# Performance work log

Measured on AMD Instinct MI355X. Metric: run time of the kernel, lower is better.

## Reference

```python
import jax, jax.numpy as jnp
import numpy as np

N_NODES = 100000
N_EDGES = 1600000
D_FEAT = 64
H1 = 16
H2 = 1


def setup_inputs() -> dict:
    key = jax.random.key(0)
    ks = jax.random.split(key, 8)
    x = jax.random.normal(ks[0], (N_NODES, D_FEAT), dtype=jnp.float32)
    edge_index = jax.random.randint(ks[1], (2, N_EDGES), 0, N_NODES, dtype=jnp.int64)
    s1 = 1.0 / np.sqrt(D_FEAT)
    s2 = 1.0 / np.sqrt(H1)
    Wl1 = jax.random.uniform(ks[2], (H1, D_FEAT), jnp.float32, -s1, s1)
    Wr1 = jax.random.uniform(ks[3], (H1, D_FEAT), jnp.float32, -s1, s1)
    b1 = jax.random.uniform(ks[4], (H1,), jnp.float32, -s1, s1)
    Wl2 = jax.random.uniform(ks[5], (H2, H1), jnp.float32, -s2, s2)
    Wr2 = jax.random.uniform(ks[6], (H2, H1), jnp.float32, -s2, s2)
    b2 = jax.random.uniform(ks[7], (H2,), jnp.float32, -s2, s2)
    return {"x": x, "edge_index": edge_index, "Wl1": Wl1, "Wr1": Wr1, "b1": b1,
            "Wl2": Wl2, "Wr2": Wr2, "b2": b2}


def _sage_conv(h, src, dst, Wl, Wr, b, n_nodes):
    # mean aggregation of source-node features onto destination nodes
    msg_sum = jax.ops.segment_sum(h[src], dst, num_segments=n_nodes)  # [N, d]
    cnt = jax.ops.segment_sum(jnp.ones((src.shape[0],), h.dtype), dst,
                              num_segments=n_nodes)  # [N]
    mean = msg_sum / jnp.maximum(cnt, 1.0)[:, None]
    # out = lin_l(mean_neighbors) + lin_r(self) + bias
    return mean @ Wl.T + h @ Wr.T + b


def reference(x, edge_index, Wl1, Wr1, b1, Wl2, Wr2, b2):
    src, dst = edge_index[0], edge_index[1]
    n = x.shape[0]
    h = jax.nn.relu(_sage_conv(x, src, dst, Wl1, Wr1, b1, n))
    # F.dropout(training=False) is identity at inference
    out = _sage_conv(h, src, dst, Wl2, Wr2, b2, n)
    return out
```

## Files before the change

### kernel.cpp

```cpp
#include <hip/hip_runtime.h>
#include <hip/hip_fp16.h>

#define H1F 16
#define BSH 8
#define BNODES 256
#define MAXBUCK 512
#define CAPSH 13
#define CAPB (1 << CAPSH)
#define SSH 10
#define TILE 4096
#define MAXPT 16

__global__ __launch_bounds__(512) void part_kernel(
    const int* __restrict__ ei,
    int* __restrict__ cur8,
    unsigned int* __restrict__ edge2,
    int E) {
    __shared__ int lhist[MAXBUCK];
    __shared__ int lbase[MAXBUCK];
    __shared__ int gbase[MAXBUCK];
    __shared__ int wsum[8];
    __shared__ unsigned int stage[TILE];
    __shared__ unsigned short sbuck[TILE];

    int t = threadIdx.x;
    int shard = blockIdx.x & 7;
    lhist[t] = 0;
    __syncthreads();

    int e0 = blockIdx.x * TILE;
    int eb = e0 + t * 8;

    int ss[8], dd[8];
    if (eb + 8 <= E) {
        int4 s0 = *(const int4*)(ei + eb);
        int4 s1 = *(const int4*)(ei + eb + 4);
        int4 d0 = *(const int4*)(ei + E + eb);
        int4 d1 = *(const int4*)(ei + E + eb + 4);
        ss[0]=s0.x; ss[1]=s0.y; ss[2]=s0.z; ss[3]=s0.w;
        ss[4]=s1.x; ss[5]=s1.y; ss[6]=s1.z; ss[7]=s1.w;
        dd[0]=d0.x; dd[1]=d0.y; dd[2]=d0.z; dd[3]=d0.w;
        dd[4]=d1.x; dd[5]=d1.y; dd[6]=d1.z; dd[7]=d1.w;
    } else {
#pragma unroll
        for (int k = 0; k < 8; ++k) {
            int e = eb + k;
            ss[k] = (e < E) ? ei[e] : -1;
            dd[k] = (e < E) ? ei[E + e] : 0;
        }
    }

    unsigned int pk[8];
    int rk[8], bk[8];
#pragma unroll
    for (int k = 0; k < 8; ++k) {
        if (ss[k] >= 0) {
            int b = dd[k] >> BSH;
            bk[k] = b;
            pk[k] = ((unsigned int)ss[k] << BSH) |
                    (unsigned int)(dd[k] & (BNODES - 1));
            rk[k] = atomicAdd(&lhist[b], 1);
        } else {
            bk[k] = -1;
        }
    }
    __syncthreads();

    int cnt = E - e0; if (cnt > TILE) cnt = TILE;

    int v = lhist[t];
    if (v > 0)
        gbase[t] = (t << CAPSH) + (shard << SSH) +
                   atomicAdd(&cur8[shard * MAXBUCK + t], v);
    int lane = t & 63, wid = t >> 6;
    int s = v;
#pragma unroll
    for (int d = 1; d < 64; d <<= 1) {
        int u = __shfl_up(s, d);
        if (lane >= d) s += u;
    }
    if (lane == 63) wsum[wid] = s;
    __syncthreads();
    int wofs = 0;
    for (int w = 0; w < wid; ++w) wofs += wsum[w];
    lbase[t] = wofs + s - v;
    __syncthreads();

#pragma unroll
    for (int k = 0; k < 8; ++k) {
        if (bk[k] >= 0) {
            int p = lbase[bk[k]] + rk[k];
            stage[p] = pk[k];
            sbuck[p] = (unsigned short)bk[k];
        }
    }
    __syncthreads();

    for (int i = t; i < cnt; i += 512) {
        int b = sbuck[i];
        int idx = gbase[b] + (i - lbase[b]);
        if (idx < (b << CAPSH) + ((shard + 1) << SSH)) edge2[idx] = stage[i];
    }
}

union SharedU {
    struct {
        int h[BNODES];
        int wsum[4];
    } s;
    struct {
        float4 wl4[16][17];
        float4 wr4[16][17];
    } q;
};

__global__ __launch_bounds__(512) void sortproj_kernel(
    const unsigned int* __restrict__ edge2,
    const int* __restrict__ cur8,
    int* __restrict__ csr,
    int* __restrict__ offp,
    int* __restrict__ degv,
    const float* __restrict__ x,
    const float* __restrict__ Wl1,
    const float* __restrict__ Wr1,
    const float* __restrict__ b1,
    __half* __restrict__ xl,
    float* __restrict__ xr,
    int N, int nSort) {
    __shared__ SharedU sh;
    int t = threadIdx.x;

    if ((int)blockIdx.x < nSort) {
        int b = blockIdx.x;
        int n0 = b << BSH;
        int e0 = b << CAPSH;

        if (t < BNODES) sh.s.h[t] = 0;
        __syncthreads();

        unsigned int rw[MAXPT];
#pragma unroll
        for (int s = 0; s < 8; ++s) {
            int cs = cur8[s * MAXBUCK + b];
            if (cs > (1 << SSH)) cs = (1 << SSH);
            int base = e0 + (s << SSH);
#pragma unroll
            for (int k = 0; k < 2; ++k) {
                int idx = (k << 9) + t;
                rw[s * 2 + k] = (idx < cs) ? edge2[base + idx] : 0xFFFFFFFFu;
            }
        }

#pragma unroll
        for (int k = 0; k < MAXPT; ++k)
            if (rw[k] != 0xFFFFFFFFu) atomicAdd(&sh.s.h[rw[k] & (BNODES - 1)], 1);
        __syncthreads();

        int lane = t & 63, wid = t >> 6;
        int v = 0, s = 0;
        if (t < BNODES) {
            v = sh.s.h[t];
            s = v;
#pragma unroll
            for (int d = 1; d < 64; d <<= 1) {
                int u = __shfl_up(s, d);
                if (lane >= d) s += u;
            }
            if (lane == 63) sh.s.wsum[wid] = s;
        }
        __syncthreads();
        if (t < BNODES) {
            int wofs = 0;
            for (int w = 0; w < wid; ++w) wofs += sh.s.wsum[w];
            int excl = wofs + s - v;
            int gn = n0 + t;
            if (gn < N) {
                degv[gn] = v;
                offp[gn] = e0 + excl;
            }
            sh.s.h[t] = excl;
        }
        __syncthreads();

#pragma unroll
        for (int k = 0; k < MAXPT; ++k) {
            if (rw[k] != 0xFFFFFFFFu) {
                int d = (int)(rw[k] & (BNODES - 1));
                int pos = atomicAdd(&sh.s.h[d], 1);
                csr[e0 + pos] = (int)(rw[k] >> BSH);
            }
        }
    } else {
        if (t < 256) {
            ((float4*)&sh.q.wl4[t >> 4][t & 15])[0] = ((const float4*)Wl1)[t];
        } else {
            int u = t - 256;
            ((float4*)&sh.q.wr4[u >> 4][u & 15])[0] = ((const float4*)Wr1)[u];
        }
        __syncthreads();

        int f = t & 15;
        int nl = t >> 4;
        float bf = b1[f];
        int blk = blockIdx.x - nSort;
        const float4* x4 = (const float4*)x;

#pragma unroll
        for (int rep = 0; rep < 4; ++rep) {
            int gn = blk * 128 + rep * 32 + nl;
            if (gn < N) {
                float al = 0.0f, ar = 0.0f;
#pragma unroll
                for (int k4 = 0; k4 < 16; ++k4) {
                    float4 xv = x4[(size_t)gn * 16 + k4];
                    float4 a = sh.q.wl4[f][k4];
                    float4 b = sh.q.wr4[f][k4];
                    al += xv.x * a.x + xv.y * a.y + xv.z * a.z + xv.w * a.w;
                    ar += xv.x * b.x + xv.y * b.y + xv.z * b.z + xv.w * b.w;
                }
                xl[(size_t)gn * H1F + f] = __float2half(al);
                xr[(size_t)gn * H1F + f] = ar + bf;
            }
        }
    }
}

__global__ void gather1_kernel(const int* __restrict__ csr,
                               const int* __restrict__ offp,
                               const int* __restrict__ degv,
                               const __half2* __restrict__ xl2,
                               const float2* __restrict__ xr2,
                               const float* __restrict__ Wl2,
                               const float* __restrict__ Wr2,
                               const float* __restrict__ b2,
                               float* __restrict__ hl2,
                               float* __restrict__ outp,
                               int N, int nbuck) {
    int g = blockIdx.x;
    int xcd = g & 7, r = g >> 3;
    int bi = r >> 3, k = r & 7;
    int b = bi * 8 + xcd;
    if (b >= nbuck) return;
    int node = (b << BSH) + (k << 5) + (threadIdx.x >> 3);
    int l = threadIdx.x & 7;
    if (node >= N) return;

    int d = degv[node];
    const int* row = csr + offp[node];

    float sx = 0.0f, sy = 0.0f;
    int j = 0;
    for (; j + 4 <= d; j += 4) {
        int s0 = row[j], s1 = row[j + 1], s2 = row[j + 2], s3 = row[j + 3];
        float2 v0 = __half22float2(xl2[(size_t)s0 * 8 + l]);
        float2 v1 = __half22float2(xl2[(size_t)s1 * 8 + l]);
        float2 v2 = __half22float2(xl2[(size_t)s2 * 8 + l]);
        float2 v3 = __half22float2(xl2[(size_t)s3 * 8 + l]);
        sx += v0.x + v1.x + v2.x + v3.x;
        sy += v0.y + v1.y + v2.y + v3.y;
    }
    for (; j < d; ++j) {
        float2 v = __half22float2(xl2[(size_t)row[j] * 8 + l]);
        sx += v.x; sy += v.y;
    }

    float inv = 1.0f / fmaxf((float)d, 1.0f);
    float2 xrv = xr2[(size_t)node * 8 + l];
    float h0 = fmaxf(sx * inv + xrv.x, 0.0f);
    float h1 = fmaxf(sy * inv + xrv.y, 0.0f);
    float2 wlv = ((const float2*)Wl2)[l];
    float2 wrv = ((const float2*)Wr2)[l];
    float pl = h0 * wlv.x + h1 * wlv.y;
    float pr = h0 * wrv.x + h1 * wrv.y;
#pragma unroll
    for (int off = 4; off; off >>= 1) {
        pl += __shfl_xor(pl, off);
        pr += __shfl_xor(pr, off);
    }
    if (l == 0) {
        hl2[node] = pl;
        outp[node] = pr + b2[0];
    }
}

__global__ void gather2_kernel(const int* __restrict__ csr,
                               const int* __restrict__ offp,
                               const int* __restrict__ degv,
                               const float* __restrict__ hl2,
                               const float* __restrict__ outp,
                               float* __restrict__ out,
                               int N, int nbuck) {
    int g = blockIdx.x;
    int xcd = g & 7, r = g >> 3;
    int bi = r >> 2, k = r & 3;
    int b = bi * 8 + xcd;
    if (b >= nbuck) return;
    int node = (b << BSH) + (k << 6) + (threadIdx.x >> 2);
    int l = threadIdx.x & 3;
    if (node >= N) return;

    int d = degv[node];
    const int* row = csr + offp[node];

    float s = 0.0f;
    for (int j = l; j < d; j += 4) s += hl2[row[j]];
    s += __shfl_xor(s, 1);
    s += __shfl_xor(s, 2);
    if (l == 0) out[node] = s / fmaxf((float)d, 1.0f) + outp[node];
}

extern "C" void kernel_launch(void* const* d_in, const int* in_sizes, int n_in,
                              void* d_out, int out_size, void* d_ws, size_t ws_size,
                              hipStream_t stream) {
    const float* x   = (const float*)d_in[0];
    const int*   ei  = (const int*)d_in[1];
    const float* Wl1 = (const float*)d_in[2];
    const float* Wr1 = (const float*)d_in[3];
    const float* b1  = (const float*)d_in[4];
    const float* Wl2 = (const float*)d_in[5];
    const float* Wr2 = (const float*)d_in[6];
    const float* b2  = (const float*)d_in[7];
    float* out = (float*)d_out;

    int N = in_sizes[0] / 64;
    int E = in_sizes[1] / 2;
    int nbuck = (N + BNODES - 1) >> BSH;

    size_t win = (size_t)nbuck << CAPSH;
    int* cur8 = (int*)d_ws;
    unsigned int* edge2 = (unsigned int*)(cur8 + 8 * MAXBUCK);
    int*   csr  = (int*)(edge2 + win);
    int*   offp = csr + win;
    int*   degv = offp + N;
    __half* xl  = (__half*)(degv + N);
    float* xr   = (float*)(xl + (size_t)16 * N);
    float* hl2  = xr + (size_t)16 * N;
    float* outp = hl2 + N;

    int nPart = (E + TILE - 1) / TILE;
    int nProj = (N + 127) / 128;

    (void)hipMemsetAsync(cur8, 0, 8 * MAXBUCK * sizeof(int), stream);

    part_kernel<<<nPart, 512, 0, stream>>>(ei, cur8, edge2, E);

    sortproj_kernel<<<nbuck + nProj, 512, 0, stream>>>(
        edge2, cur8, csr, offp, degv,
        x, Wl1, Wr1, b1, xl, xr, N, nbuck);

    int grid1 = 8 * ((nbuck + 7) / 8) * 8;
    gather1_kernel<<<grid1, 256, 0, stream>>>(
        csr, offp, degv, (const __half2*)xl, (const float2*)xr,
        Wl2, Wr2, b2, hl2, outp, N, nbuck);

    int grid2 = 8 * ((nbuck + 7) / 8) * 4;
    gather2_kernel<<<grid2, 256, 0, stream>>>(
        csr, offp, degv, hl2, outp, out, N, nbuck);
}
```

Baseline: 70.95 us.

## Co-schedule projection with partition and simplify gather block mapping

The dense layer-1 projection moves out of the sort kernel and into the partition kernel, so partition and projection blocks share one launch and the sort kernel runs only bucket sorting. The gather kernels drop the XCD-aware bucket swizzle, use plain linear node indexing and grow from 256 to 512 threads per block. All kernels now take a single Params struct. The shared-memory union now includes the partition staging buffers, which raises LDS use for the projection blocks, and losing the XCD locality mapping may change L2 behaviour.

```diff
diff --git a/kernel.cpp b/kernel.cpp
--- a/kernel.cpp
+++ b/kernel.cpp
@@ -6,37 +6,58 @@
 #define BNODES 256
 #define MAXBUCK 512
 #define CAPSH 13
-#define CAPB (1 << CAPSH)
 #define SSH 10
 #define TILE 4096
 #define MAXPT 16
 
-__global__ __launch_bounds__(512) void part_kernel(
-    const int* __restrict__ ei,
-    int* __restrict__ cur8,
-    unsigned int* __restrict__ edge2,
-    int E) {
-    __shared__ int lhist[MAXBUCK];
-    __shared__ int lbase[MAXBUCK];
-    __shared__ int gbase[MAXBUCK];
-    __shared__ int wsum[8];
-    __shared__ unsigned int stage[TILE];
-    __shared__ unsigned short sbuck[TILE];
-
-    int t = threadIdx.x;
-    int shard = blockIdx.x & 7;
-    lhist[t] = 0;
-    __syncthreads();
-
-    int e0 = blockIdx.x * TILE;
+struct Params {
+    const float* x;
+    const float* Wl1; const float* Wr1; const float* b1;
+    const float* Wl2; const float* Wr2; const float* b2;
+    const int* ei;
+    int* cur8;
+    unsigned int* edge2;
+    int* csr; int* offp; int* degv;
+    __half* xl; float* xr; float* hl2; float* outp;
+    float* out;
+    int N, E, nPart, nProj, nbuck;
+};
+
+union SharedU {
+    struct {
+        int lhist[MAXBUCK];
+        int lbase[MAXBUCK];
+        int gbase[MAXBUCK];
+        int wsum[8];
+        unsigned int stage[TILE];
+        unsigned short sbuck[TILE];
+    } p;
+    struct {
+        float4 wl4[16][17];
+        float4 wr4[16][17];
+    } q;
+    struct {
+        int h[BNODES];
+        int wsum[4];
+    } s;
+};
+
+__device__ __forceinline__ void do_part(const Params& P, int vb, SharedU& sh) {
+    int t = threadIdx.x;
+    int shard = vb & 7;
+    sh.p.lhist[t] = 0;
+    __syncthreads();
+
+    int E = P.E;
+    int e0 = vb * TILE;
     int eb = e0 + t * 8;
 
     int ss[8], dd[8];
     if (eb + 8 <= E) {
-        int4 s0 = *(const int4*)(ei + eb);
-        int4 s1 = *(const int4*)(ei + eb + 4);
-        int4 d0 = *(const int4*)(ei + E + eb);
-        int4 d1 = *(const int4*)(ei + E + eb + 4);
+        int4 s0 = *(const int4*)(P.ei + eb);
+        int4 s1 = *(const int4*)(P.ei + eb + 4);
+        int4 d0 = *(const int4*)(P.ei + E + eb);
+        int4 d1 = *(const int4*)(P.ei + E + eb + 4);
         ss[0]=s0.x; ss[1]=s0.y; ss[2]=s0.z; ss[3]=s0.w;
         ss[4]=s1.x; ss[5]=s1.y; ss[6]=s1.z; ss[7]=s1.w;
         dd[0]=d0.x; dd[1]=d0.y; dd[2]=d0.z; dd[3]=d0.w;
@@ -45,8 +66,8 @@
 #pragma unroll
         for (int k = 0; k < 8; ++k) {
             int e = eb + k;
-            ss[k] = (e < E) ? ei[e] : -1;
-            dd[k] = (e < E) ? ei[E + e] : 0;
+            ss[k] = (e < E) ? P.ei[e] : -1;
+            dd[k] = (e < E) ? P.ei[E + e] : 0;
         }
     }
 
@@ -59,7 +80,7 @@
             bk[k] = b;
             pk[k] = ((unsigned int)ss[k] << BSH) |
                     (unsigned int)(dd[k] & (BNODES - 1));
-            rk[k] = atomicAdd(&lhist[b], 1);
+            rk[k] = atomicAdd(&sh.p.lhist[b], 1);
         } else {
             bk[k] = -1;
         }
@@ -68,10 +89,10 @@
 
     int cnt = E - e0; if (cnt > TILE) cnt = TILE;
 
-    int v = lhist[t];
+    int v = sh.p.lhist[t];
     if (v > 0)
-        gbase[t] = (t << CAPSH) + (shard << SSH) +
-                   atomicAdd(&cur8[shard * MAXBUCK + t], v);
+        sh.p.gbase[t] = (t << CAPSH) + (shard << SSH) +
+                        atomicAdd(&P.cur8[shard * MAXBUCK + t], v);
     int lane = t & 63, wid = t >> 6;
     int s = v;
 #pragma unroll
@@ -79,174 +100,138 @@
         int u = __shfl_up(s, d);
         if (lane >= d) s += u;
     }
-    if (lane == 63) wsum[wid] = s;
+    if (lane == 63) sh.p.wsum[wid] = s;
     __syncthreads();
     int wofs = 0;
-    for (int w = 0; w < wid; ++w) wofs += wsum[w];
-    lbase[t] = wofs + s - v;
+    for (int w = 0; w < wid; ++w) wofs += sh.p.wsum[w];
+    sh.p.lbase[t] = wofs + s - v;
     __syncthreads();
 
 #pragma unroll
     for (int k = 0; k < 8; ++k) {
         if (bk[k] >= 0) {
-            int p = lbase[bk[k]] + rk[k];
-            stage[p] = pk[k];
-            sbuck[p] = (unsigned short)bk[k];
+            int p = sh.p.lbase[bk[k]] + rk[k];
+            sh.p.stage[p] = pk[k];
+            sh.p.sbuck[p] = (unsigned short)bk[k];
         }
     }
     __syncthreads();
 
     for (int i = t; i < cnt; i += 512) {
-        int b = sbuck[i];
-        int idx = gbase[b] + (i - lbase[b]);
-        if (idx < (b << CAPSH) + ((shard + 1) << SSH)) edge2[idx] = stage[i];
-    }
-}
-
-union SharedU {
-    struct {
-        int h[BNODES];
-        int wsum[4];
-    } s;
-    struct {
-        float4 wl4[16][17];
-        float4 wr4[16][17];
-    } q;
-};
-
-__global__ __launch_bounds__(512) void sortproj_kernel(
-    const unsigned int* __restrict__ edge2,
-    const int* __restrict__ cur8,
-    int* __restrict__ csr,
-    int* __restrict__ offp,
-    int* __restrict__ degv,
-    const float* __restrict__ x,
-    const float* __restrict__ Wl1,
-    const float* __restrict__ Wr1,
-    const float* __restrict__ b1,
-    __half* __restrict__ xl,
-    float* __restrict__ xr,
-    int N, int nSort) {
-    __shared__ SharedU sh;
-    int t = threadIdx.x;
-
-    if ((int)blockIdx.x < nSort) {
-        int b = blockIdx.x;
-        int n0 = b << BSH;
-        int e0 = b << CAPSH;
-
-        if (t < BNODES) sh.s.h[t] = 0;
-        __syncthreads();
-
-        unsigned int rw[MAXPT];
-#pragma unroll
-        for (int s = 0; s < 8; ++s) {
-            int cs = cur8[s * MAXBUCK + b];
-            if (cs > (1 << SSH)) cs = (1 << SSH);
-            int base = e0 + (s << SSH);
-#pragma unroll
-            for (int k = 0; k < 2; ++k) {
-                int idx = (k << 9) + t;
-                rw[s * 2 + k] = (idx < cs) ? edge2[base + idx] : 0xFFFFFFFFu;
+        int b = sh.p.sbuck[i];
+        int idx = sh.p.gbase[b] + (i - sh.p.lbase[b]);
+        int shardEnd = (b << CAPSH) + ((shard + 1) << SSH);
+        if (idx < shardEnd) P.edge2[idx] = sh.p.stage[i];
+    }
+}
+
+__device__ __forceinline__ void do_proj(const Params& P, int pvb, SharedU& sh) {
+    int t = threadIdx.x;
+    if (t < 256) {
+        sh.q.wl4[t >> 4][t & 15] = ((const float4*)P.Wl1)[t];
+    } else {
+        int u = t - 256;
+        sh.q.wr4[u >> 4][u & 15] = ((const float4*)P.Wr1)[u];
+    }
+    __syncthreads();
+
+    int f = t & 15;
+    int nl = t >> 4;
+    float bf = P.b1[f];
+    const float4* x4 = (const float4*)P.x;
+
+#pragma unroll
+    for (int rep = 0; rep < 4; ++rep) {
+        int gn = pvb * 128 + rep * 32 + nl;
+        if (gn < P.N) {
+            float al = 0.0f, ar = 0.0f;
+#pragma unroll
+            for (int k4 = 0; k4 < 16; ++k4) {
+                float4 xv = x4[(size_t)gn * 16 + k4];
+                float4 a = sh.q.wl4[f][k4];
+                float4 b = sh.q.wr4[f][k4];
+                al += xv.x * a.x + xv.y * a.y + xv.z * a.z + xv.w * a.w;
+                ar += xv.x * b.x + xv.y * b.y + xv.z * b.z + xv.w * b.w;
             }
-        }
-
-#pragma unroll
-        for (int k = 0; k < MAXPT; ++k)
-            if (rw[k] != 0xFFFFFFFFu) atomicAdd(&sh.s.h[rw[k] & (BNODES - 1)], 1);
-        __syncthreads();
-
-        int lane = t & 63, wid = t >> 6;
-        int v = 0, s = 0;
-        if (t < BNODES) {
-            v = sh.s.h[t];
-            s = v;
-#pragma unroll
-            for (int d = 1; d < 64; d <<= 1) {
-                int u = __shfl_up(s, d);
-                if (lane >= d) s += u;
-            }
-            if (lane == 63) sh.s.wsum[wid] = s;
-        }
-        __syncthreads();
-        if (t < BNODES) {
-            int wofs = 0;
-            for (int w = 0; w < wid; ++w) wofs += sh.s.wsum[w];
-            int excl = wofs + s - v;
-            int gn = n0 + t;
-            if (gn < N) {
-                degv[gn] = v;
-                offp[gn] = e0 + excl;
-            }
-            sh.s.h[t] = excl;
-        }
-        __syncthreads();
-
-#pragma unroll
-        for (int k = 0; k < MAXPT; ++k) {
-            if (rw[k] != 0xFFFFFFFFu) {
-                int d = (int)(rw[k] & (BNODES - 1));
-                int pos = atomicAdd(&sh.s.h[d], 1);
-                csr[e0 + pos] = (int)(rw[k] >> BSH);
-            }
-        }
-    } else {
-        if (t < 256) {
-            ((float4*)&sh.q.wl4[t >> 4][t & 15])[0] = ((const float4*)Wl1)[t];
-        } else {
-            int u = t - 256;
-            ((float4*)&sh.q.wr4[u >> 4][u & 15])[0] = ((const float4*)Wr1)[u];
-        }
-        __syncthreads();
-
-        int f = t & 15;
-        int nl = t >> 4;
-        float bf = b1[f];
-        int blk = blockIdx.x - nSort;
-        const float4* x4 = (const float4*)x;
-
-#pragma unroll
-        for (int rep = 0; rep < 4; ++rep) {
-            int gn = blk * 128 + rep * 32 + nl;
-            if (gn < N) {
-                float al = 0.0f, ar = 0.0f;
-#pragma unroll
-                for (int k4 = 0; k4 < 16; ++k4) {
-                    float4 xv = x4[(size_t)gn * 16 + k4];
-                    float4 a = sh.q.wl4[f][k4];
-                    float4 b = sh.q.wr4[f][k4];
-                    al += xv.x * a.x + xv.y * a.y + xv.z * a.z + xv.w * a.w;
-                    ar += xv.x * b.x + xv.y * b.y + xv.z * b.z + xv.w * b.w;
-                }
-                xl[(size_t)gn * H1F + f] = __float2half(al);
-                xr[(size_t)gn * H1F + f] = ar + bf;
-            }
-        }
-    }
-}
-
-__global__ void gather1_kernel(const int* __restrict__ csr,
-                               const int* __restrict__ offp,
-                               const int* __restrict__ degv,
-                               const __half2* __restrict__ xl2,
-                               const float2* __restrict__ xr2,
-                               const float* __restrict__ Wl2,
-                               const float* __restrict__ Wr2,
-                               const float* __restrict__ b2,
-                               float* __restrict__ hl2,
-                               float* __restrict__ outp,
-                               int N, int nbuck) {
-    int g = blockIdx.x;
-    int xcd = g & 7, r = g >> 3;
-    int bi = r >> 3, k = r & 7;
-    int b = bi * 8 + xcd;
-    if (b >= nbuck) return;
-    int node = (b << BSH) + (k << 5) + (threadIdx.x >> 3);
-    int l = threadIdx.x & 7;
-    if (node >= N) return;
-
-    int d = degv[node];
-    const int* row = csr + offp[node];
+            P.xl[(size_t)gn * H1F + f] = __float2half(al);
+            P.xr[(size_t)gn * H1F + f] = ar + bf;
+        }
+    }
+}
+
+__device__ __forceinline__ void do_sort(const Params& P, int b, SharedU& sh) {
+    int t = threadIdx.x;
+    int n0 = b << BSH;
+    int e0 = b << CAPSH;
+
+    if (t < BNODES) sh.s.h[t] = 0;
+    __syncthreads();
+
+    unsigned int rw[MAXPT];
+#pragma unroll
+    for (int s = 0; s < 8; ++s) {
+        int cs = P.cur8[s * MAXBUCK + b];
+        if (cs > (1 << SSH)) cs = (1 << SSH);
+        int base = e0 + (s << SSH);
+#pragma unroll
+        for (int k = 0; k < 2; ++k) {
+            int idx = (k << 9) + t;
+            rw[s * 2 + k] = (idx < cs) ? P.edge2[base + idx] : 0xFFFFFFFFu;
+        }
+    }
+
+#pragma unroll
+    for (int k = 0; k < MAXPT; ++k)
+        if (rw[k] != 0xFFFFFFFFu) atomicAdd(&sh.s.h[rw[k] & (BNODES - 1)], 1);
+    __syncthreads();
+
+    int lane = t & 63, wid = t >> 6;
+    int v = 0, s = 0;
+    if (t < BNODES) {
+        v = sh.s.h[t];
+        s = v;
+#pragma unroll
+        for (int d = 1; d < 64; d <<= 1) {
+            int u = __shfl_up(s, d);
+            if (lane >= d) s += u;
+        }
+        if (lane == 63) sh.s.wsum[wid] = s;
+    }
+    __syncthreads();
+    if (t < BNODES) {
+        int wofs = 0;
+        for (int w = 0; w < wid; ++w) wofs += sh.s.wsum[w];
+        int excl = wofs + s - v;
+        int gn = n0 + t;
+        if (gn < P.N) {
+            P.degv[gn] = v;
+            P.offp[gn] = e0 + excl;
+        }
+        sh.s.h[t] = excl;
+    }
+    __syncthreads();
+
+#pragma unroll
+    for (int k = 0; k < MAXPT; ++k) {
+        if (rw[k] != 0xFFFFFFFFu) {
+            int d = (int)(rw[k] & (BNODES - 1));
+            int pos = atomicAdd(&sh.s.h[d], 1);
+            P.csr[e0 + pos] = (int)(rw[k] >> BSH);
+        }
+    }
+}
+
+__device__ __forceinline__ void do_gather1(const Params& P, int vb) {
+    int t = threadIdx.x;
+    int node = vb * 64 + (t >> 3);
+    int l = t & 7;
+    if (node >= P.N) return;
+
+    const __half2* xl2 = (const __half2*)P.xl;
+    const float2* xr2 = (const float2*)P.xr;
+
+    int d = P.degv[node];
+    const int* row = P.csr + P.offp[node];
 
     float sx = 0.0f, sy = 0.0f;
     int j = 0;
@@ -268,8 +253,8 @@
     float2 xrv = xr2[(size_t)node * 8 + l];
     float h0 = fmaxf(sx * inv + xrv.x, 0.0f);
     float h1 = fmaxf(sy * inv + xrv.y, 0.0f);
-    float2 wlv = ((const float2*)Wl2)[l];
-    float2 wrv = ((const float2*)Wr2)[l];
+    float2 wlv = ((const float2*)P.Wl2)[l];
+    float2 wrv = ((const float2*)P.Wr2)[l];
     float pl = h0 * wlv.x + h1 * wlv.y;
     float pr = h0 * wrv.x + h1 * wrv.y;
 #pragma unroll
@@ -278,82 +263,75 @@
         pr += __shfl_xor(pr, off);
     }
     if (l == 0) {
-        hl2[node] = pl;
-        outp[node] = pr + b2[0];
-    }
-}
-
-__global__ void gather2_kernel(const int* __restrict__ csr,
-                               const int* __restrict__ offp,
-                               const int* __restrict__ degv,
-                               const float* __restrict__ hl2,
-                               const float* __restrict__ outp,
-                               float* __restrict__ out,
-                               int N, int nbuck) {
-    int g = blockIdx.x;
-    int xcd = g & 7, r = g >> 3;
-    int bi = r >> 2, k = r & 3;
-    int b = bi * 8 + xcd;
-    if (b >= nbuck) return;
-    int node = (b << BSH) + (k << 6) + (threadIdx.x >> 2);
-    int l = threadIdx.x & 3;
-    if (node >= N) return;
-
-    int d = degv[node];
-    const int* row = csr + offp[node];
+        P.hl2[node] = pl;
+        P.outp[node] = pr + P.b2[0];
+    }
+}
+
+__device__ __forceinline__ void do_gather2(const Params& P, int vb) {
+    int t = threadIdx.x;
+    int node = vb * 128 + (t >> 2);
+    int l = t & 3;
+    if (node >= P.N) return;
+
+    int d = P.degv[node];
+    const int* row = P.csr + P.offp[node];
 
     float s = 0.0f;
-    for (int j = l; j < d; j += 4) s += hl2[row[j]];
+    for (int j = l; j < d; j += 4) s += P.hl2[row[j]];
     s += __shfl_xor(s, 1);
     s += __shfl_xor(s, 2);
-    if (l == 0) out[node] = s / fmaxf((float)d, 1.0f) + outp[node];
-}
+    if (l == 0) P.out[node] = s / fmaxf((float)d, 1.0f) + P.outp[node];
+}
+
+__global__ __launch_bounds__(512) void kA(Params P) {
+    __shared__ SharedU sh;
+    int vb = blockIdx.x;
+    if (vb < P.nPart) do_part(P, vb, sh);
+    else do_proj(P, vb - P.nPart, sh);
+}
+__global__ __launch_bounds__(512) void kB(Params P) {
+    __shared__ SharedU sh;
+    do_sort(P, blockIdx.x, sh);
+}
+__global__ __launch_bounds__(512) void kC(Params P) { do_gather1(P, blockIdx.x); }
+__global__ __launch_bounds__(512) void kD(Params P) { do_gather2(P, blockIdx.x); }
 
 extern "C" void kernel_launch(void* const* d_in, const int* in_sizes, int n_in,
                               void* d_out, int out_size, void* d_ws, size_t ws_size,
                               hipStream_t stream) {
-    const float* x   = (const float*)d_in[0];
-    const int*   ei  = (const int*)d_in[1];
-    const float* Wl1 = (const float*)d_in[2];
-    const float* Wr1 = (const float*)d_in[3];
-    const float* b1  = (const float*)d_in[4];
-    const float* Wl2 = (const float*)d_in[5];
-    const float* Wr2 = (const float*)d_in[6];
-    const float* b2  = (const float*)d_in[7];
-    float* out = (float*)d_out;
-
-    int N = in_sizes[0] / 64;
-    int E = in_sizes[1] / 2;
-    int nbuck = (N + BNODES - 1) >> BSH;
-
-    size_t win = (size_t)nbuck << CAPSH;
-    int* cur8 = (int*)d_ws;
-    unsigned int* edge2 = (unsigned int*)(cur8 + 8 * MAXBUCK);
-    int*   csr  = (int*)(edge2 + win);
-    int*   offp = csr + win;
-    int*   degv = offp + N;
-    __half* xl  = (__half*)(degv + N);
-    float* xr   = (float*)(xl + (size_t)16 * N);
-    float* hl2  = xr + (size_t)16 * N;
-    float* outp = hl2 + N;
-
-    int nPart = (E + TILE - 1) / TILE;
-    int nProj = (N + 127) / 128;
-
-    (void)hipMemsetAsync(cur8, 0, 8 * MAXBUCK * sizeof(int), stream);
-
-    part_kernel<<<nPart, 512, 0, stream>>>(ei, cur8, edge2, E);
-
-    sortproj_kernel<<<nbuck + nProj, 512, 0, stream>>>(
-        edge2, cur8, csr, offp, degv,
-        x, Wl1, Wr1, b1, xl, xr, N, nbuck);
-
-    int grid1 = 8 * ((nbuck + 7) / 8) * 8;
-    gather1_kernel<<<grid1, 256, 0, stream>>>(
-        csr, offp, degv, (const __half2*)xl, (const float2*)xr,
-        Wl2, Wr2, b2, hl2, outp, N, nbuck);
-
-    int grid2 = 8 * ((nbuck + 7) / 8) * 4;
-    gather2_kernel<<<grid2, 256, 0, stream>>>(
-        csr, offp, degv, hl2, outp, out, N, nbuck);
-}
+    Params P;
+    P.x   = (const float*)d_in[0];
+    P.ei  = (const int*)d_in[1];
+    P.Wl1 = (const float*)d_in[2];
+    P.Wr1 = (const float*)d_in[3];
+    P.b1  = (const float*)d_in[4];
+    P.Wl2 = (const float*)d_in[5];
+    P.Wr2 = (const float*)d_in[6];
+    P.b2  = (const float*)d_in[7];
+    P.out = (float*)d_out;
+
+    P.N = in_sizes[0] / 64;
+    P.E = in_sizes[1] / 2;
+    P.nbuck = (P.N + BNODES - 1) >> BSH;
+    P.nPart = (P.E + TILE - 1) / TILE;
+    P.nProj = (P.N + 127) / 128;
+
+    size_t win = (size_t)P.nbuck << CAPSH;
+    P.cur8  = (int*)d_ws;
+    P.edge2 = (unsigned int*)(P.cur8 + 8 * MAXBUCK);
+    P.csr   = (int*)(P.edge2 + win);
+    P.offp  = P.csr + win;
+    P.degv  = P.offp + P.N;
+    P.xl    = (__half*)(P.degv + P.N);
+    P.xr    = (float*)(P.xl + (size_t)16 * P.N);
+    P.hl2   = P.xr + (size_t)16 * P.N;
+    P.outp  = P.hl2 + P.N;
+
+    (void)hipMemsetAsync(P.cur8, 0, 8 * MAXBUCK * sizeof(int), stream);
+
+    kA<<<P.nPart + P.nProj, 512, 0, stream>>>(P);
+    kB<<<P.nbuck, 512, 0, stream>>>(P);
+    kC<<<(P.N + 63) / 64, 512, 0, stream>>>(P);
+    kD<<<(P.N + 127) / 128, 512, 0, stream>>>(P);
+}
```

Result: slower. 76.83 us (+8.3%).
